# Performance work log

Measured on AMD Instinct MI355X. Metric: run time of the kernel, lower is better.

Reference implementation:

```python
import jax, jax.numpy as jnp
import numpy as np

N_NODES = 80000
N_EDGES = 1280000
IN_CH = 128
HID = 64
N_GRAPHS = 64
DROPOUT_P = 0.3


def setup_inputs() -> dict:
    key = jax.random.key(0)
    ks = jax.random.split(key, 12)
    x = jax.random.normal(ks[0], (N_NODES, IN_CH), dtype=jnp.float32)
    edge_index = jax.random.randint(ks[1], (2, N_EDGES), 0, N_NODES, dtype=jnp.int64 if jax.config.read('jax_enable_x64') else jnp.int32)
    batch = jnp.sort(jax.random.randint(ks[2], (N_NODES,), 0, N_GRAPHS))
    def lin(k, fan_in, fan_out):
        lim = 1.0 / np.sqrt(fan_in)
        kw, kb = jax.random.split(k)
        W = jax.random.uniform(kw, (fan_in, fan_out), minval=-lim, maxval=lim, dtype=jnp.float32)
        b = jax.random.uniform(kb, (fan_out,), minval=-lim, maxval=lim, dtype=jnp.float32)
        return W, b
    W1, b1 = lin(ks[3], IN_CH, HID)
    W2, b2 = lin(ks[4], HID, HID)
    W3, b3 = lin(ks[5], HID, HID)
    Wm1, bm1 = lin(ks[6], HID, HID)
    Wm2, bm2 = lin(ks[7], HID, 1)
    return {"x": x, "edge_index": edge_index, "batch": batch,
            "W1": W1, "b1": b1, "W2": W2, "b2": b2, "W3": W3, "b3": b3,
            "Wm1": Wm1, "bm1": bm1, "Wm2": Wm2, "bm2": bm2}


def _gcn_conv(x, W, b, src, dst, deg_inv_sqrt):
    # PyG GCNConv: h = X W; add self-loops; norm_e = d^-1/2[src] * d^-1/2[dst]
    h = x @ W  # [N, F]
    norm = deg_inv_sqrt[src] * deg_inv_sqrt[dst]  # [E]
    agg = jax.ops.segment_sum(h[src] * norm[:, None], dst, num_segments=x.shape[0])
    agg = agg + h * (deg_inv_sqrt * deg_inv_sqrt)[:, None]  # self-loop term d^-1
    return agg + b


def _dropout(x, key, p):
    keep = jax.random.bernoulli(key, 1.0 - p, x.shape)
    return jnp.where(keep, x / (1.0 - p), 0.0)


def reference(x, edge_index, batch, W1, b1, W2, b2, W3, b3, Wm1, bm1, Wm2, bm2):
    src, dst = edge_index[0], edge_index[1]
    N = x.shape[0]
    # in-degree on dst, +1 for self-loop (PyG default normalization)
    deg = jax.ops.segment_sum(jnp.ones_like(dst, dtype=x.dtype), dst, num_segments=N) + 1.0
    deg_inv_sqrt = jax.lax.rsqrt(deg)

    dk = jax.random.split(jax.random.key(42), 4)
    h = _dropout(jax.nn.relu(_gcn_conv(x, W1, b1, src, dst, deg_inv_sqrt)), dk[0], DROPOUT_P)
    h = _dropout(jax.nn.relu(_gcn_conv(h, W2, b2, src, dst, deg_inv_sqrt)), dk[1], DROPOUT_P)
    h = _dropout(jax.nn.relu(_gcn_conv(h, W3, b3, src, dst, deg_inv_sqrt)), dk[2], DROPOUT_P)

    # global mean pool per graph
    sums = jax.ops.segment_sum(h, batch, num_segments=N_GRAPHS)
    counts = jax.ops.segment_sum(jnp.ones((N,), dtype=h.dtype), batch, num_segments=N_GRAPHS)
    pooled = sums / jnp.maximum(counts, 1.0)[:, None]  # [G, HID]

    # MLP head: Linear -> ReLU -> Dropout -> Linear
    m = jax.nn.relu(pooled @ Wm1 + bm1)
    m = _dropout(m, dk[3], DROPOUT_P)
    return m @ Wm2 + bm2  # [G, 1]
```

## Files before the change

### kernel.cpp

```cpp
#include <hip/hip_runtime.h>
#include <hip/hip_fp8.h>
#include <stdint.h>

#define HID 64
#define INCH 128
#define NGRAPH 64
#define KEEPP 0.7f
#define SCAN_B 256

typedef __attribute__((ext_vector_type(8))) short short8;
typedef __attribute__((ext_vector_type(4))) float floatx4;
typedef unsigned short ushort_t;

__device__ __forceinline__ uint8_t f2e4(float f) {
  __hip_fp8_e4m3 t(f);
  return (uint8_t)t.__x;
}
__device__ __forceinline__ float e42f(uint8_t b) {
  __hip_fp8_e4m3 t;
  t.__x = (__hip_fp8_storage_t)b;
  return (float)t;
}

__host__ __device__ inline void tf2x32(uint32_t k0, uint32_t k1,
                                       uint32_t& x0, uint32_t& x1) {
  const uint32_t ks2 = k0 ^ k1 ^ 0x1BD11BDAu;
#define ROTL32(v, d) (((v) << (d)) | ((v) >> (32 - (d))))
#define TF_RND(r) { x0 += x1; x1 = ROTL32(x1, r); x1 ^= x0; }
  x0 += k0; x1 += k1;
  TF_RND(13) TF_RND(15) TF_RND(26) TF_RND(6)
  x0 += k1;  x1 += ks2 + 1u;
  TF_RND(17) TF_RND(29) TF_RND(16) TF_RND(24)
  x0 += ks2; x1 += k0 + 2u;
  TF_RND(13) TF_RND(15) TF_RND(26) TF_RND(6)
  x0 += k0;  x1 += k1 + 3u;
  TF_RND(17) TF_RND(29) TF_RND(16) TF_RND(24)
  x0 += k1;  x1 += ks2 + 4u;
  TF_RND(13) TF_RND(15) TF_RND(26) TF_RND(6)
  x0 += ks2; x1 += k0 + 5u;
#undef TF_RND
#undef ROTL32
}

__device__ __forceinline__ bool keep_mask(uint32_t k0, uint32_t k1, uint32_t idx) {
  uint32_t x0 = 0u, x1 = idx;
  tf2x32(k0, k1, x0, x1);
  uint32_t bits = x0 ^ x1;
  float u = __uint_as_float((bits >> 9) | 0x3f800000u) - 1.0f;
  return u < KEEPP;
}

__global__ void k_hist(const int* __restrict__ dst, int E, int* __restrict__ counts) {
  int e = blockIdx.x * blockDim.x + threadIdx.x;
  if (e < E) atomicAdd(&counts[dst[e]], 1);
}

__global__ __launch_bounds__(SCAN_B) void k_scan1d(const int* __restrict__ counts,
                                                   int* __restrict__ bsum,
                                                   float* __restrict__ dinv, int N) {
  int i = blockIdx.x * SCAN_B + threadIdx.x;
  int v = 0;
  if (i < N) {
    v = counts[i];
    dinv[i] = rsqrtf((float)v + 1.0f);
  }
  int r = v;
  for (int off = 32; off > 0; off >>= 1) r += __shfl_down(r, off);
  __shared__ int ws[4];
  if ((threadIdx.x & 63) == 0) ws[threadIdx.x >> 6] = r;
  __syncthreads();
  if (threadIdx.x == 0) bsum[blockIdx.x] = ws[0] + ws[1] + ws[2] + ws[3];
}

__device__ __forceinline__ void wsplit_one(const float* __restrict__ W,
                                           short8* __restrict__ Wh,
                                           short8* __restrict__ Wl, int i) {
  int lane = i & 63, f = i >> 6;
  int kc = f >> 2, ct = f & 3;
  int kbase = kc * 32 + ((lane >> 4) << 3);
  int n = ct * 16 + (lane & 15);
  short8 h, l;
#pragma unroll
  for (int j = 0; j < 8; ++j) {
    float w = W[(size_t)(kbase + j) * HID + n];
    uint32_t u = __float_as_uint(w);
    h[j] = (short)(u >> 16);
    float r = w - __uint_as_float(u & 0xFFFF0000u);
    l[j] = (short)(__float_as_uint(r) >> 16);
  }
  Wh[i] = h;
  Wl[i] = l;
}

__global__ __launch_bounds__(1024) void k_scan2w(const int* __restrict__ bsum,
                                                 int* __restrict__ bpre, int B,
                                                 const float* __restrict__ W1,
                                                 short8* __restrict__ Wh1, short8* __restrict__ Wl1,
                                                 const float* __restrict__ W2,
                                                 short8* __restrict__ Wh2, short8* __restrict__ Wl2,
                                                 const float* __restrict__ W3,
                                                 short8* __restrict__ Wh3, short8* __restrict__ Wl3) {
  if (blockIdx.x == 0) {
    __shared__ int s[1024];
    int tid = threadIdx.x;
    int v = (tid < B) ? bsum[tid] : 0;
    s[tid] = v;
    __syncthreads();
    for (int off = 1; off < 1024; off <<= 1) {
      int t = (tid >= off) ? s[tid - off] : 0;
      __syncthreads();
      s[tid] += t;
      __syncthreads();
    }
    if (tid < B) bpre[tid] = s[tid] - v;
    return;
  }
  int b = blockIdx.x - 1;
  int tid = threadIdx.x;
  if (b == 0) {
    wsplit_one(W1, Wh1, Wl1, tid);
  } else if (b == 1 && tid < 512) {
    wsplit_one(W2, Wh2, Wl2, tid);
  } else if (b == 2 && tid < 512) {
    wsplit_one(W3, Wh3, Wl3, tid);
  }
}

__global__ __launch_bounds__(SCAN_B) void k_scan3(const int* __restrict__ counts,
                                                  const int* __restrict__ bpre,
                                                  int* __restrict__ row_off,
                                                  int* __restrict__ cursor,
                                                  int N, int E) {
  __shared__ int s[SCAN_B];
  int tid = threadIdx.x;
  int i = blockIdx.x * SCAN_B + tid;
  int v = (i < N) ? counts[i] : 0;
  s[tid] = v;
  __syncthreads();
  for (int off = 1; off < SCAN_B; off <<= 1) {
    int t = (tid >= off) ? s[tid - off] : 0;
    __syncthreads();
    s[tid] += t;
    __syncthreads();
  }
  if (i < N) {
    int excl = bpre[blockIdx.x] + s[tid] - v;
    row_off[i] = excl;
    cursor[i] = excl;
  }
  if (i == 0) row_off[N] = E;
}

template <int K>
__device__ __forceinline__ void mgemm_tile(const float* __restrict__ A,
                                           const short8* __restrict__ Wh,
                                           const short8* __restrict__ Wl,
                                           uint8_t* __restrict__ C, int N,
                                           int tile) {
  constexpr int KC = K / 32;
  const int lane = threadIdx.x & 63;
  const int wv = threadIdx.x >> 6;
  const int m = lane & 15;
  const int q = lane >> 4;
  const int row0 = tile * 64 + wv * 16;
  if (row0 >= N) return;
  const int arow = min(row0 + m, N - 1);
  const float* __restrict__ ap = A + (size_t)arow * K + (q << 3);

  floatx4 acc[4];
#pragma unroll
  for (int ct = 0; ct < 4; ++ct) acc[ct] = (floatx4){0.f, 0.f, 0.f, 0.f};

#pragma unroll
  for (int kc = 0; kc < KC; ++kc) {
    const floatx4* apv = (const floatx4*)(ap + kc * 32);
    floatx4 x0 = apv[0];
    floatx4 x1 = apv[1];
    short8 ah, al;
#pragma unroll
    for (int j = 0; j < 4; ++j) {
      uint32_t u = __float_as_uint(x0[j]);
      ah[j] = (short)(u >> 16);
      float r = x0[j] - __uint_as_float(u & 0xFFFF0000u);
      al[j] = (short)(__float_as_uint(r) >> 16);
    }
#pragma unroll
    for (int j = 0; j < 4; ++j) {
      uint32_t u = __float_as_uint(x1[j]);
      ah[4 + j] = (short)(u >> 16);
      float r = x1[j] - __uint_as_float(u & 0xFFFF0000u);
      al[4 + j] = (short)(__float_as_uint(r) >> 16);
    }
#pragma unroll
    for (int ct = 0; ct < 4; ++ct) {
      short8 bh = Wh[(kc * 4 + ct) * 64 + lane];
      short8 bl = Wl[(kc * 4 + ct) * 64 + lane];
      acc[ct] = __builtin_amdgcn_mfma_f32_16x16x32_bf16(ah, bh, acc[ct], 0, 0, 0);
      acc[ct] = __builtin_amdgcn_mfma_f32_16x16x32_bf16(ah, bl, acc[ct], 0, 0, 0);
      acc[ct] = __builtin_amdgcn_mfma_f32_16x16x32_bf16(al, bh, acc[ct], 0, 0, 0);
    }
  }

  uint8_t* __restrict__ cp = C + (size_t)row0 * HID;
#pragma unroll
  for (int ct = 0; ct < 4; ++ct)
#pragma unroll
    for (int r = 0; r < 4; ++r) {
      int rr = (q << 2) + r;
      if (row0 + rr < N) cp[(size_t)rr * HID + ct * 16 + m] = f2e4(acc[ct][r]);
    }
}

template <int K>
__global__ __launch_bounds__(256) void k_mgemm_build(
    const float* __restrict__ A, const short8* __restrict__ Wh,
    const short8* __restrict__ Wl, uint8_t* __restrict__ C, int N,
    const int* __restrict__ src, const int* __restrict__ dst,
    const float* __restrict__ dinv, int* __restrict__ cursor,
    int2* __restrict__ csr, int E, int build_blocks, int gemm_blocks) {
  const long T = (long)build_blocks + gemm_blocks;
  const long b = (long)blockIdx.x;
  const long gb = (b * gemm_blocks) / T;
  const bool is_g = (((b + 1) * gemm_blocks) / T) != gb;
  if (!is_g) {
    int bb = (int)(b - gb);
    int e = bb * 256 + (int)threadIdx.x;
    if (e < E) {
      int s = src[e], d = dst[e];
      int pos = atomicAdd(&cursor[d], 1);
      csr[pos] = make_int2(s, __float_as_int(dinv[s] * dinv[d]));
    }
    return;
  }
  mgemm_tile<K>(A, Wh, Wl, C, N, (int)gb);
}

template <int K>
__global__ __launch_bounds__(256) void k_mgemm(const float* __restrict__ A,
                                               const short8* __restrict__ Wh,
                                               const short8* __restrict__ Wl,
                                               uint8_t* __restrict__ C, int N) {
  mgemm_tile<K>(A, Wh, Wl, C, N, (int)blockIdx.x);
}

__global__ __launch_bounds__(256) void k_gather(const uint8_t* __restrict__ tmp,
                                                const int* __restrict__ row_off,
                                                const int2* __restrict__ csr,
                                                const float* __restrict__ dinv,
                                                const float* __restrict__ bias,
                                                float* __restrict__ outh, int N,
                                                uint32_t k0, uint32_t k1) {
  const int node = blockIdx.x * 4 + (threadIdx.x >> 6);
  const int lane = threadIdx.x & 63;
  const int q = lane >> 4;
  const int sl = lane & 15;
  if (node >= N) return;
  const int beg = __builtin_amdgcn_readfirstlane(row_off[node]);
  const int end = __builtin_amdgcn_readfirstlane(row_off[node + 1]);

  float a0 = 0.f, a1 = 0.f, a2 = 0.f, a3 = 0.f;
  for (int j = beg; j < end; j += 8) {
    int e0 = j + q, e1 = j + 4 + q;
    bool v0 = e0 < end, v1 = e1 < end;
    int2 p0 = csr[v0 ? e0 : beg];
    int2 p1 = csr[v1 ? e1 : beg];
    float w0 = v0 ? __int_as_float(p0.y) : 0.0f;
    float w1 = v1 ? __int_as_float(p1.y) : 0.0f;
    uint32_t r0 = *(const uint32_t*)(tmp + (size_t)p0.x * HID + sl * 4);
    uint32_t r1 = *(const uint32_t*)(tmp + (size_t)p1.x * HID + sl * 4);
    a0 = fmaf(e42f((uint8_t)(r0      )), w0, a0);
    a1 = fmaf(e42f((uint8_t)(r0 >>  8)), w0, a1);
    a2 = fmaf(e42f((uint8_t)(r0 >> 16)), w0, a2);
    a3 = fmaf(e42f((uint8_t)(r0 >> 24)), w0, a3);
    a0 = fmaf(e42f((uint8_t)(r1      )), w1, a0);
    a1 = fmaf(e42f((uint8_t)(r1 >>  8)), w1, a1);
    a2 = fmaf(e42f((uint8_t)(r1 >> 16)), w1, a2);
    a3 = fmaf(e42f((uint8_t)(r1 >> 24)), w1, a3);
  }
  a0 += __shfl_xor(a0, 16); a0 += __shfl_xor(a0, 32);
  a1 += __shfl_xor(a1, 16); a1 += __shfl_xor(a1, 32);
  a2 += __shfl_xor(a2, 16); a2 += __shfl_xor(a2, 32);
  a3 += __shfl_xor(a3, 16); a3 += __shfl_xor(a3, 32);
  float acc = (q == 0) ? a0 : (q == 1) ? a1 : (q == 2) ? a2 : a3;
  const int ch = sl * 4 + q;
  const float dnode = dinv[node];
  const int idx = node * HID + ch;
  float v = acc + e42f(tmp[(size_t)node * HID + ch]) * dnode * dnode + bias[ch];
  v = fmaxf(v, 0.0f);
  v = keep_mask(k0, k1, (uint32_t)idx) ? v / KEEPP : 0.0f;
  outh[idx] = v;
}

__global__ __launch_bounds__(256) void k_pool(const float* __restrict__ h,
                                              const int* __restrict__ batch,
                                              float* __restrict__ sums,
                                              float* __restrict__ cnts, int N) {
  __shared__ float ls[NGRAPH * HID];
  __shared__ float lc[NGRAPH];
  for (int i = threadIdx.x; i < NGRAPH * HID; i += 256) ls[i] = 0.0f;
  if (threadIdx.x < NGRAPH) lc[threadIdx.x] = 0.0f;
  __syncthreads();
  const int lane = threadIdx.x & 63;
  const int wave = threadIdx.x >> 6;
  int per = (N + gridDim.x - 1) / gridDim.x;
  int beg = blockIdx.x * per;
  int end = min(N, beg + per);
  for (int i = beg + wave; i < end; i += 4) {
    int g = batch[i];
    atomicAdd(&ls[g * HID + lane], h[(size_t)i * HID + lane]);
    if (lane == 0) atomicAdd(&lc[g], 1.0f);
  }
  __syncthreads();
  for (int i = threadIdx.x; i < NGRAPH * HID; i += 256)
    if (ls[i] != 0.0f) atomicAdd(&sums[i], ls[i]);
  if (threadIdx.x < NGRAPH && lc[threadIdx.x] != 0.0f)
    atomicAdd(&cnts[threadIdx.x], lc[threadIdx.x]);
}

__global__ __launch_bounds__(256) void k_head(const float* __restrict__ sums,
                                              const float* __restrict__ cnts,
                                              const float* __restrict__ Wm1,
                                              const float* __restrict__ bm1,
                                              const float* __restrict__ Wm2,
                                              const float* __restrict__ bm2,
                                              float* __restrict__ out,
                                              uint32_t k0, uint32_t k1) {
  __shared__ float pooled[NGRAPH * HID];
  __shared__ float m[NGRAPH * HID];
  for (int i = threadIdx.x; i < NGRAPH * HID; i += 256) {
    int g = i >> 6;
    pooled[i] = sums[i] / fmaxf(cnts[g], 1.0f);
  }
  __syncthreads();
  for (int i = threadIdx.x; i < NGRAPH * HID; i += 256) {
    int g = i >> 6, j = i & 63;
    float acc = bm1[j];
#pragma unroll 8
    for (int k = 0; k < HID; ++k)
      acc = fmaf(pooled[g * HID + k], Wm1[k * HID + j], acc);
    acc = fmaxf(acc, 0.0f);
    m[i] = keep_mask(k0, k1, (uint32_t)i) ? acc / KEEPP : 0.0f;
  }
  __syncthreads();
  if (threadIdx.x < NGRAPH) {
    int g = threadIdx.x;
    float acc = bm2[0];
#pragma unroll 8
    for (int j = 0; j < HID; ++j)
      acc = fmaf(m[g * HID + j], Wm2[j], acc);
    out[g] = acc;
  }
}

extern "C" void kernel_launch(void* const* d_in, const int* in_sizes, int n_in,
                              void* d_out, int out_size, void* d_ws, size_t ws_size,
                              hipStream_t stream) {
  const float* x     = (const float*)d_in[0];
  const int*   ei    = (const int*)d_in[1];
  const int*   batch = (const int*)d_in[2];
  const float* W1 = (const float*)d_in[3];
  const float* b1 = (const float*)d_in[4];
  const float* W2 = (const float*)d_in[5];
  const float* b2 = (const float*)d_in[6];
  const float* W3 = (const float*)d_in[7];
  const float* b3 = (const float*)d_in[8];
  const float* Wm1 = (const float*)d_in[9];
  const float* bm1 = (const float*)d_in[10];
  const float* Wm2 = (const float*)d_in[11];
  const float* bm2 = (const float*)d_in[12];
  float* out = (float*)d_out;

  const int N = in_sizes[0] / INCH;
  const int E = in_sizes[1] / 2;
  const int* src = ei;
  const int* dst = ei + E;
  const int NB = (N + SCAN_B - 1) / SCAN_B;

  char* ws = (char*)d_ws;
  size_t off = 0;
  uint8_t* B0 = (uint8_t*)(ws + off); off += (size_t)N * HID;
  off = (off + 15) & ~(size_t)15;
  float* B1      = (float*)(ws + off); off += (size_t)N * HID * 4;
  float* dinv    = (float*)(ws + off); off += (size_t)N * 4;
  int*   counts  = (int*)  (ws + off); off += (size_t)N * 4;
  int*   row_off = (int*)  (ws + off); off += ((size_t)N + 4) * 4;
  int*   cursor  = (int*)  (ws + off); off += (size_t)N * 4;
  int*   bsum    = (int*)  (ws + off); off += 1024 * 4;
  int*   bpre    = (int*)  (ws + off); off += 1024 * 4;
  int2*  csr     = (int2*) (ws + off); off += (size_t)E * 8;
  float* sums    = (float*)(ws + off); off += NGRAPH * HID * 4;
  float* cnts    = (float*)(ws + off); off += NGRAPH * 4;
  off = (off + 15) & ~(size_t)15;
  short8* Wh1 = (short8*)(ws + off); off += 1024 * 16;
  short8* Wl1 = (short8*)(ws + off); off += 1024 * 16;
  short8* Wh2 = (short8*)(ws + off); off += 512 * 16;
  short8* Wl2 = (short8*)(ws + off); off += 512 * 16;
  short8* Wh3 = (short8*)(ws + off); off += 512 * 16;
  short8* Wl3 = (short8*)(ws + off); off += 512 * 16;

  uint32_t dk[4][2];
  for (uint32_t i = 0; i < 4; ++i) {
    uint32_t a = 0u, b = i;
    tf2x32(0u, 42u, a, b);
    dk[i][0] = a; dk[i][1] = b;
  }

  hipMemsetAsync(counts, 0, (size_t)N * sizeof(int), stream);
  k_hist<<<(E + 255) / 256, 256, 0, stream>>>(dst, E, counts);
  k_scan1d<<<NB, SCAN_B, 0, stream>>>(counts, bsum, dinv, N);
  k_scan2w<<<4, 1024, 0, stream>>>(bsum, bpre, NB,
                                   W1, Wh1, Wl1, W2, Wh2, Wl2, W3, Wh3, Wl3);
  k_scan3<<<NB, SCAN_B, 0, stream>>>(counts, bpre, row_off, cursor, N, E);

  const int build_grid = (E + 255) / 256;
  const int mg_grid    = (N + 63) / 64;
  const int gath_grid  = (N + 3) / 4;

  k_mgemm_build<INCH><<<build_grid + mg_grid, 256, 0, stream>>>(
      x, Wh1, Wl1, B0, N, src, dst, dinv, cursor, csr, E, build_grid, mg_grid);
  k_gather<<<gath_grid, 256, 0, stream>>>(B0, row_off, csr, dinv, b1,
                                          B1, N, dk[0][0], dk[0][1]);
  k_mgemm<HID><<<mg_grid, 256, 0, stream>>>(B1, Wh2, Wl2, B0, N);
  k_gather<<<gath_grid, 256, 0, stream>>>(B0, row_off, csr, dinv, b2,
                                          B1, N, dk[1][0], dk[1][1]);
  k_mgemm<HID><<<mg_grid, 256, 0, stream>>>(B1, Wh3, Wl3, B0, N);
  k_gather<<<gath_grid, 256, 0, stream>>>(B0, row_off, csr, dinv, b3,
                                          B1, N, dk[2][0], dk[2][1]);

  hipMemsetAsync(sums, 0, (NGRAPH * HID + NGRAPH) * sizeof(float), stream);
  k_pool<<<256, 256, 0, stream>>>(B1, batch, sums, cnts, N);
  k_head<<<1, 256, 0, stream>>>(sums, cnts, Wm1, bm1, Wm2, bm2, out,
                                dk[3][0], dk[3][1]);
  (void)n_in; (void)out_size; (void)ws_size;
}
```

Before: 418.4 us.

## Fuse mean-pool into last gather, use packed fp8 convert, fold count/zero setup

The third-layer gather now accumulates its activated, dropped-out outputs straight into per-graph sums with global float atomics. This removes the write of the final hidden buffer, the separate pool kernel and a memset. Per-graph node counts move into the degree-scan kernel, and the sums zeroing moves into the block-scan kernel. The gather inner loop uses the packed fp8-to-f32 conversion builtin when it is available. The risk is heavy atomic contention: every node does 64 global atomics, and because the batch is sorted, neighbouring nodes hit the same few addresses.

```diff
diff --git a/kernel.cpp b/kernel.cpp
--- a/kernel.cpp
+++ b/kernel.cpp
@@ -10,6 +10,7 @@
 
 typedef __attribute__((ext_vector_type(8))) short short8;
 typedef __attribute__((ext_vector_type(4))) float floatx4;
+typedef __attribute__((ext_vector_type(2))) float floatx2;
 typedef unsigned short ushort_t;
 
 __device__ __forceinline__ uint8_t f2e4(float f) {
@@ -20,6 +21,20 @@
   __hip_fp8_e4m3 t;
   t.__x = (__hip_fp8_storage_t)b;
   return (float)t;
+}
+
+__device__ __forceinline__ void e42f_x4(uint32_t r, float& f0, float& f1,
+                                        float& f2, float& f3) {
+#if __has_builtin(__builtin_amdgcn_cvt_pk_f32_fp8)
+  floatx2 lo = __builtin_amdgcn_cvt_pk_f32_fp8((int)r, false);
+  floatx2 hi = __builtin_amdgcn_cvt_pk_f32_fp8((int)r, true);
+  f0 = lo.x; f1 = lo.y; f2 = hi.x; f3 = hi.y;
+#else
+  f0 = e42f((uint8_t)(r      ));
+  f1 = e42f((uint8_t)(r >>  8));
+  f2 = e42f((uint8_t)(r >> 16));
+  f3 = e42f((uint8_t)(r >> 24));
+#endif
 }
 
 __host__ __device__ inline void tf2x32(uint32_t k0, uint32_t k1,
@@ -57,12 +72,18 @@
 
 __global__ __launch_bounds__(SCAN_B) void k_scan1d(const int* __restrict__ counts,
                                                    int* __restrict__ bsum,
-                                                   float* __restrict__ dinv, int N) {
+                                                   float* __restrict__ dinv,
+                                                   const int* __restrict__ batch,
+                                                   float* __restrict__ cnts, int N) {
+  __shared__ int lh[NGRAPH];
+  if (threadIdx.x < NGRAPH) lh[threadIdx.x] = 0;
+  __syncthreads();
   int i = blockIdx.x * SCAN_B + threadIdx.x;
   int v = 0;
   if (i < N) {
     v = counts[i];
     dinv[i] = rsqrtf((float)v + 1.0f);
+    atomicAdd(&lh[batch[i]], 1);
   }
   int r = v;
   for (int off = 32; off > 0; off >>= 1) r += __shfl_down(r, off);
@@ -70,6 +91,8 @@
   if ((threadIdx.x & 63) == 0) ws[threadIdx.x >> 6] = r;
   __syncthreads();
   if (threadIdx.x == 0) bsum[blockIdx.x] = ws[0] + ws[1] + ws[2] + ws[3];
+  if (threadIdx.x < NGRAPH && lh[threadIdx.x] != 0)
+    atomicAdd(&cnts[threadIdx.x], (float)lh[threadIdx.x]);
 }
 
 __device__ __forceinline__ void wsplit_one(const float* __restrict__ W,
@@ -94,6 +117,7 @@
 
 __global__ __launch_bounds__(1024) void k_scan2w(const int* __restrict__ bsum,
                                                  int* __restrict__ bpre, int B,
+                                                 float* __restrict__ sums,
                                                  const float* __restrict__ W1,
                                                  short8* __restrict__ Wh1, short8* __restrict__ Wl1,
                                                  const float* __restrict__ W2,
@@ -103,6 +127,7 @@
   if (blockIdx.x == 0) {
     __shared__ int s[1024];
     int tid = threadIdx.x;
+    for (int i = tid; i < NGRAPH * HID; i += 1024) sums[i] = 0.0f;
     int v = (tid < B) ? bsum[tid] : 0;
     s[tid] = v;
     __syncthreads();
@@ -243,6 +268,34 @@
   mgemm_tile<K>(A, Wh, Wl, C, N, (int)blockIdx.x);
 }
 
+__device__ __forceinline__ float gather_core(const uint8_t* __restrict__ tmp,
+                                             const int2* __restrict__ csr,
+                                             int beg, int end, int q, int sl) {
+  float a0 = 0.f, a1 = 0.f, a2 = 0.f, a3 = 0.f;
+  for (int j = beg; j < end; j += 8) {
+    int e0 = j + q, e1 = j + 4 + q;
+    bool v0 = e0 < end, v1 = e1 < end;
+    int2 p0 = csr[v0 ? e0 : beg];
+    int2 p1 = csr[v1 ? e1 : beg];
+    float w0 = v0 ? __int_as_float(p0.y) : 0.0f;
+    float w1 = v1 ? __int_as_float(p1.y) : 0.0f;
+    uint32_t r0 = *(const uint32_t*)(tmp + (size_t)p0.x * HID + sl * 4);
+    uint32_t r1 = *(const uint32_t*)(tmp + (size_t)p1.x * HID + sl * 4);
+    float f0, f1, f2, f3, g0, g1, g2, g3;
+    e42f_x4(r0, f0, f1, f2, f3);
+    e42f_x4(r1, g0, g1, g2, g3);
+    a0 = fmaf(f0, w0, a0); a1 = fmaf(f1, w0, a1);
+    a2 = fmaf(f2, w0, a2); a3 = fmaf(f3, w0, a3);
+    a0 = fmaf(g0, w1, a0); a1 = fmaf(g1, w1, a1);
+    a2 = fmaf(g2, w1, a2); a3 = fmaf(g3, w1, a3);
+  }
+  a0 += __shfl_xor(a0, 16); a0 += __shfl_xor(a0, 32);
+  a1 += __shfl_xor(a1, 16); a1 += __shfl_xor(a1, 32);
+  a2 += __shfl_xor(a2, 16); a2 += __shfl_xor(a2, 32);
+  a3 += __shfl_xor(a3, 16); a3 += __shfl_xor(a3, 32);
+  return (q == 0) ? a0 : (q == 1) ? a1 : (q == 2) ? a2 : a3;
+}
+
 __global__ __launch_bounds__(256) void k_gather(const uint8_t* __restrict__ tmp,
                                                 const int* __restrict__ row_off,
                                                 const int2* __restrict__ csr,
@@ -257,31 +310,7 @@
   if (node >= N) return;
   const int beg = __builtin_amdgcn_readfirstlane(row_off[node]);
   const int end = __builtin_amdgcn_readfirstlane(row_off[node + 1]);
-
-  float a0 = 0.f, a1 = 0.f, a2 = 0.f, a3 = 0.f;
-  for (int j = beg; j < end; j += 8) {
-    int e0 = j + q, e1 = j + 4 + q;
-    bool v0 = e0 < end, v1 = e1 < end;
-    int2 p0 = csr[v0 ? e0 : beg];
-    int2 p1 = csr[v1 ? e1 : beg];
-    float w0 = v0 ? __int_as_float(p0.y) : 0.0f;
-    float w1 = v1 ? __int_as_float(p1.y) : 0.0f;
-    uint32_t r0 = *(const uint32_t*)(tmp + (size_t)p0.x * HID + sl * 4);
-    uint32_t r1 = *(const uint32_t*)(tmp + (size_t)p1.x * HID + sl * 4);
-    a0 = fmaf(e42f((uint8_t)(r0      )), w0, a0);
-    a1 = fmaf(e42f((uint8_t)(r0 >>  8)), w0, a1);
-    a2 = fmaf(e42f((uint8_t)(r0 >> 16)), w0, a2);
-    a3 = fmaf(e42f((uint8_t)(r0 >> 24)), w0, a3);
-    a0 = fmaf(e42f((uint8_t)(r1      )), w1, a0);
-    a1 = fmaf(e42f((uint8_t)(r1 >>  8)), w1, a1);
-    a2 = fmaf(e42f((uint8_t)(r1 >> 16)), w1, a2);
-    a3 = fmaf(e42f((uint8_t)(r1 >> 24)), w1, a3);
-  }
-  a0 += __shfl_xor(a0, 16); a0 += __shfl_xor(a0, 32);
-  a1 += __shfl_xor(a1, 16); a1 += __shfl_xor(a1, 32);
-  a2 += __shfl_xor(a2, 16); a2 += __shfl_xor(a2, 32);
-  a3 += __shfl_xor(a3, 16); a3 += __shfl_xor(a3, 32);
-  float acc = (q == 0) ? a0 : (q == 1) ? a1 : (q == 2) ? a2 : a3;
+  float acc = gather_core(tmp, csr, beg, end, q, sl);
   const int ch = sl * 4 + q;
   const float dnode = dinv[node];
   const int idx = node * HID + ch;
@@ -291,30 +320,30 @@
   outh[idx] = v;
 }
 
-__global__ __launch_bounds__(256) void k_pool(const float* __restrict__ h,
-                                              const int* __restrict__ batch,
-                                              float* __restrict__ sums,
-                                              float* __restrict__ cnts, int N) {
-  __shared__ float ls[NGRAPH * HID];
-  __shared__ float lc[NGRAPH];
-  for (int i = threadIdx.x; i < NGRAPH * HID; i += 256) ls[i] = 0.0f;
-  if (threadIdx.x < NGRAPH) lc[threadIdx.x] = 0.0f;
-  __syncthreads();
+__global__ __launch_bounds__(256) void k_gather_pool(const uint8_t* __restrict__ tmp,
+                                                     const int* __restrict__ row_off,
+                                                     const int2* __restrict__ csr,
+                                                     const float* __restrict__ dinv,
+                                                     const float* __restrict__ bias,
+                                                     const int* __restrict__ batch,
+                                                     float* __restrict__ sums, int N,
+                                                     uint32_t k0, uint32_t k1) {
+  const int node = blockIdx.x * 4 + (threadIdx.x >> 6);
   const int lane = threadIdx.x & 63;
-  const int wave = threadIdx.x >> 6;
-  int per = (N + gridDim.x - 1) / gridDim.x;
-  int beg = blockIdx.x * per;
-  int end = min(N, beg + per);
-  for (int i = beg + wave; i < end; i += 4) {
-    int g = batch[i];
-    atomicAdd(&ls[g * HID + lane], h[(size_t)i * HID + lane]);
-    if (lane == 0) atomicAdd(&lc[g], 1.0f);
-  }
-  __syncthreads();
-  for (int i = threadIdx.x; i < NGRAPH * HID; i += 256)
-    if (ls[i] != 0.0f) atomicAdd(&sums[i], ls[i]);
-  if (threadIdx.x < NGRAPH && lc[threadIdx.x] != 0.0f)
-    atomicAdd(&cnts[threadIdx.x], lc[threadIdx.x]);
+  const int q = lane >> 4;
+  const int sl = lane & 15;
+  if (node >= N) return;
+  const int beg = __builtin_amdgcn_readfirstlane(row_off[node]);
+  const int end = __builtin_amdgcn_readfirstlane(row_off[node + 1]);
+  float acc = gather_core(tmp, csr, beg, end, q, sl);
+  const int ch = sl * 4 + q;
+  const float dnode = dinv[node];
+  const int idx = node * HID + ch;
+  float v = acc + e42f(tmp[(size_t)node * HID + ch]) * dnode * dnode + bias[ch];
+  v = fmaxf(v, 0.0f);
+  v = keep_mask(k0, k1, (uint32_t)idx) ? v / KEEPP : 0.0f;
+  const int g = __builtin_amdgcn_readfirstlane(batch[node]);
+  atomicAdd(&sums[g * HID + ch], v);
 }
 
 __global__ __launch_bounds__(256) void k_head(const float* __restrict__ sums,
@@ -381,15 +410,15 @@
   uint8_t* B0 = (uint8_t*)(ws + off); off += (size_t)N * HID;
   off = (off + 15) & ~(size_t)15;
   float* B1      = (float*)(ws + off); off += (size_t)N * HID * 4;
+  int*   counts  = (int*)  (ws + off); off += (size_t)N * 4;
+  float* cnts    = (float*)(ws + off); off += NGRAPH * 4;
   float* dinv    = (float*)(ws + off); off += (size_t)N * 4;
-  int*   counts  = (int*)  (ws + off); off += (size_t)N * 4;
   int*   row_off = (int*)  (ws + off); off += ((size_t)N + 4) * 4;
   int*   cursor  = (int*)  (ws + off); off += (size_t)N * 4;
   int*   bsum    = (int*)  (ws + off); off += 1024 * 4;
   int*   bpre    = (int*)  (ws + off); off += 1024 * 4;
   int2*  csr     = (int2*) (ws + off); off += (size_t)E * 8;
   float* sums    = (float*)(ws + off); off += NGRAPH * HID * 4;
-  float* cnts    = (float*)(ws + off); off += NGRAPH * 4;
   off = (off + 15) & ~(size_t)15;
   short8* Wh1 = (short8*)(ws + off); off += 1024 * 16;
   short8* Wl1 = (short8*)(ws + off); off += 1024 * 16;
@@ -405,10 +434,10 @@
     dk[i][0] = a; dk[i][1] = b;
   }
 
-  hipMemsetAsync(counts, 0, (size_t)N * sizeof(int), stream);
+  hipMemsetAsync(counts, 0, ((size_t)N + NGRAPH) * sizeof(int), stream);
   k_hist<<<(E + 255) / 256, 256, 0, stream>>>(dst, E, counts);
-  k_scan1d<<<NB, SCAN_B, 0, stream>>>(counts, bsum, dinv, N);
-  k_scan2w<<<4, 1024, 0, stream>>>(bsum, bpre, NB,
+  k_scan1d<<<NB, SCAN_B, 0, stream>>>(counts, bsum, dinv, batch, cnts, N);
+  k_scan2w<<<4, 1024, 0, stream>>>(bsum, bpre, NB, sums,
                                    W1, Wh1, Wl1, W2, Wh2, Wl2, W3, Wh3, Wl3);
   k_scan3<<<NB, SCAN_B, 0, stream>>>(counts, bpre, row_off, cursor, N, E);
 
@@ -424,11 +453,9 @@
   k_gather<<<gath_grid, 256, 0, stream>>>(B0, row_off, csr, dinv, b2,
                                           B1, N, dk[1][0], dk[1][1]);
   k_mgemm<HID><<<mg_grid, 256, 0, stream>>>(B1, Wh3, Wl3, B0, N);
-  k_gather<<<gath_grid, 256, 0, stream>>>(B0, row_off, csr, dinv, b3,
-                                          B1, N, dk[2][0], dk[2][1]);
-
-  hipMemsetAsync(sums, 0, (NGRAPH * HID + NGRAPH) * sizeof(float), stream);
-  k_pool<<<256, 256, 0, stream>>>(B1, batch, sums, cnts, N);
+  k_gather_pool<<<gath_grid, 256, 0, stream>>>(B0, row_off, csr, dinv, b3,
+                                               batch, sums, N, dk[2][0], dk[2][1]);
+
   k_head<<<1, 256, 0, stream>>>(sums, cnts, Wm1, bm1, Wm2, bm2, out,
                                 dk[3][0], dk[3][1]);
   (void)n_in; (void)out_size; (void)ws_size;
```

After: 517.7 us. +23.7%, slower.
